# Performance work log

Hardware: AMD Instinct MI355X
Metric: run time of the kernel (lower is better)

## Reference

```python
import jax, jax.numpy as jnp
import numpy as np

K_NN = 9  # kernel_size: neighbors per node (includes self, dist 0)


def knn_edges(feat):
    """feat: (B, C, N). Replicates DenseDilatedKnnGraph (dilation=1):
    L2-normalize over channels, dense pairwise sq-distance, top-k nearest."""
    nrm = jnp.sqrt(jnp.sum(feat * feat, axis=1, keepdims=True))
    xn = feat / jnp.maximum(nrm, 1e-12)            # F.normalize(dim=1)
    xt = jnp.swapaxes(xn, 1, 2)                    # (B, N, C)
    sq = jnp.sum(xt * xt, axis=-1)                 # (B, N)
    dist = sq[:, :, None] + sq[:, None, :] - 2.0 * jnp.einsum('bnc,bmc->bnm', xt, xt)
    _, nn_idx = jax.lax.top_k(-dist, K_NN)         # (B, N, k)
    center = jnp.broadcast_to(jnp.arange(nn_idx.shape[1], dtype=nn_idx.dtype)[None, :, None], nn_idx.shape)
    return nn_idx, center                          # (x_j sources, x_i targets)


def reference(x, W0, W1, bias):
    B, C, H, W = x.shape
    N = H * W
    NB = B * N
    feat = x.reshape(B, C, N)
    # KNN graph is built on detached features in the torch source
    x_j, x_i = knn_edges(jax.lax.stop_gradient(feat))
    E = B * N * K_NN
    # faithful to source: torch.linspace(0, B, steps=E, dtype=int64) batch offsets
    count = jnp.linspace(0.0, float(B), E).astype(jnp.int32)
    src = x_j.reshape(-1).astype(jnp.int32) + count * N
    dst = x_i.reshape(-1).astype(jnp.int32) + count * N
    valid = (src < NB) & (dst < NB)                # drop the out-of-range tail edge
    # flat_nodes: (B, C, H, W) -> (B*H*W, C), node id = b*HW + pixel
    nodes = jnp.swapaxes(feat, 1, 2).reshape(NB, C)
    # ChebConv K=2, sym norm, lambda_max=2: Tx0 = x, Tx1 = -(D^-1/2 A D^-1/2) x
    w = valid.astype(nodes.dtype)
    deg = jax.ops.segment_sum(w, src, num_segments=NB)
    dinv = jnp.where(deg > 0, jax.lax.rsqrt(jnp.maximum(deg, 1.0)), 0.0)
    norm = -(dinv[src] * w * dinv[dst])            # scaled-Laplacian edge weights
    msg = norm[:, None] * nodes[src]               # (E, C) gather + weight
    Tx1 = jax.ops.segment_sum(msg, dst, num_segments=NB)
    return nodes @ W0 + Tx1 @ W1 + bias


def setup_inputs() -> dict:
    key = jax.random.key(0)
    k1, k2, k3, k4 = jax.random.split(key, 4)
    B, C, H, W = 8, 48, 64, 64
    Cout = 48
    s = 1.0 / np.sqrt(C)
    return {
        'x': jax.random.normal(k1, (B, C, H, W), dtype=jnp.float32),
        'W0': jax.random.normal(k2, (C, Cout), dtype=jnp.float32) * s,
        'W1': jax.random.normal(k3, (C, Cout), dtype=jnp.float32) * s,
        'bias': jax.random.normal(k4, (Cout,), dtype=jnp.float32) * 0.01,
    }
```

## Files before the change

### kernel.cpp

```cpp
#include <hip/hip_runtime.h>

#define BATCH 8
#define CH    48
#define NPTS  4096
#define NBN   (BATCH*NPTS)
#define KNN   9
#define NCAND 12

typedef unsigned short u16;
typedef unsigned int   u32;
typedef unsigned long long u64;
typedef __bf16 bf16x8 __attribute__((ext_vector_type(8)));
typedef float  f32x4  __attribute__((ext_vector_type(4)));

__device__ __forceinline__ float bf2f(u16 v) { return __uint_as_float(((u32)v) << 16); }
__device__ __forceinline__ u16 f2bf(float f) {
  u32 u = __float_as_uint(f);
  u = (u + 0x7fffu + ((u >> 16) & 1u)) >> 16;
  return (u16)u;
}

#define MED3U(d, a, b, c) \
  asm("v_med3_u32 %0, %1, %2, %3" : "=v"(d) : "v"(a), "v"(b), "v"(c))
#define INS12(p0,p1,p2,p3,p4,p5,p6,p7,p8,p9,p10,p11,x) do { \
  MED3U(p11,p10,p11,x); MED3U(p10,p9,p10,x); MED3U(p9,p8,p9,x);  \
  MED3U(p8, p7, p8, x); MED3U(p7, p6,p7, x); MED3U(p6,p5,p6,x);  \
  MED3U(p5, p4, p5, x); MED3U(p4, p3,p4, x); MED3U(p3,p2,p3,x);  \
  MED3U(p2, p1, p2, x); MED3U(p1, p0,p1, x); p0 = min(p0, x);    \
} while (0)

__device__ __forceinline__ void stage_q(const u16* g, u16* l) {
  __builtin_amdgcn_global_load_lds(
      (const __attribute__((address_space(1))) void*)g,
      (__attribute__((address_space(3))) void*)l, 16, 0, 0);
}

__global__ __launch_bounds__(64)
void k_prep(const float* __restrict__ x, float* __restrict__ xraw,
            float* __restrict__ xn, float* __restrict__ csq,
            u16* __restrict__ Abuf, u16* __restrict__ Bbuf,
            int* __restrict__ deg) {
  int node = blockIdx.x * 64 + threadIdx.x;
  deg[node] = 0;
  int b = node >> 12, n = node & (NPTS - 1);
  const float* xb = x + (size_t)b * CH * NPTS;
  float f[CH];
#pragma unroll
  for (int c = 0; c < CH; ++c) f[c] = xb[(size_t)c * NPTS + n];
  float a0 = 0, a1 = 0, a2 = 0, a3 = 0;
#pragma unroll
  for (int k = 0; k < CH; k += 4) {
    a0 += f[k] * f[k]; a1 += f[k+1] * f[k+1];
    a2 += f[k+2] * f[k+2]; a3 += f[k+3] * f[k+3];
  }
  float nrm = fmaxf(sqrtf((a0 + a1) + (a2 + a3)), 1e-12f);
  float rn = 1.0f / nrm;
  a0 = a1 = a2 = a3 = 0;
#pragma unroll
  for (int k = 0; k < CH; k += 4) {
    float v0 = f[k]*rn, v1 = f[k+1]*rn, v2 = f[k+2]*rn, v3 = f[k+3]*rn;
    a0 += v0*v0; a1 += v1*v1; a2 += v2*v2; a3 += v3*v3;
  }
  float csqv = (a0 + a1) + (a2 + a3);
  csq[node] = csqv;
  float4* ro = (float4*)(xraw + (size_t)node * CH);
  float4* no = (float4*)(xn   + (size_t)node * CH);
#pragma unroll
  for (int i = 0; i < CH / 4; ++i) {
    ro[i] = make_float4(f[4*i], f[4*i+1], f[4*i+2], f[4*i+3]);
    no[i] = make_float4(f[4*i]*rn, f[4*i+1]*rn, f[4*i+2]*rn, f[4*i+3]*rn);
  }
  uint4* Bo = (uint4*)(Bbuf + (size_t)node * 128);
  u16* Ag = Abuf + (size_t)(node >> 4) * 2048 + (size_t)(node & 15) * 8;
#pragma unroll
  for (int g = 0; g < 6; ++g) {
    u32 bhw[4], blw[4], ahw[4], alw[4];
#pragma unroll
    for (int j = 0; j < 4; ++j) {
      int k = g * 8 + j * 2;
      float v0 = f[k] * rn, v1 = f[k+1] * rn;
      u16 h0 = f2bf(v0), h1 = f2bf(v1);
      u16 l0 = f2bf(v0 - bf2f(h0)), l1 = f2bf(v1 - bf2f(h1));
      bhw[j] = (u32)h0 | ((u32)h1 << 16);
      blw[j] = (u32)l0 | ((u32)l1 << 16);
      float w0 = -2.0f * v0, w1 = -2.0f * v1;
      u16 g0 = f2bf(w0), g1 = f2bf(w1);
      u16 m0 = f2bf(w0 - bf2f(g0)), m1 = f2bf(w1 - bf2f(g1));
      ahw[j] = (u32)g0 | ((u32)g1 << 16);
      alw[j] = (u32)m0 | ((u32)m1 << 16);
    }
    Bo[g]     = make_uint4(bhw[0], bhw[1], bhw[2], bhw[3]);
    Bo[8 + g] = make_uint4(blw[0], blw[1], blw[2], blw[3]);
    int v = g >> 2, q = g & 3;
    *(uint4*)(Ag + v * 512 + q * 128)        = make_uint4(ahw[0], ahw[1], ahw[2], ahw[3]);
    *(uint4*)(Ag + 1024 + v * 512 + q * 128) = make_uint4(alw[0], alw[1], alw[2], alw[3]);
  }
  {
    u16 h = f2bf(csqv); u16 l = f2bf(csqv - bf2f(h));
    Bo[6]  = make_uint4(0x3F80u, 0, 0, 0);
    Bo[14] = make_uint4(0, 0, 0, 0);
    *(uint4*)(Ag + 512 + 2 * 128)        = make_uint4((u32)h, 0, 0, 0);
    *(uint4*)(Ag + 1024 + 512 + 2 * 128) = make_uint4((u32)l, 0, 0, 0);
  }
  {
    uint4 z = make_uint4(0, 0, 0, 0);
    Bo[7] = z; Bo[15] = z;
    *(uint4*)(Ag + 512 + 3 * 128)        = z;
    *(uint4*)(Ag + 1024 + 512 + 3 * 128) = z;
  }
}

__global__ __launch_bounds__(256, 6)
void k_knn_m(const u16* __restrict__ Abuf, const u16* __restrict__ Bbuf,
             u32* __restrict__ candu) {
  __shared__ __align__(16) u16 As[2][2][2048];
  int tid = threadIdx.x;
  int lane = tid & 63;
  int wv = tid >> 6;
  int quad = lane >> 4, m16 = lane & 15;
  int panel = blockIdx.x * 4 + wv;
  int row = panel * 16 + m16;
  int b4096 = row & ~(NPTS - 1);
  int half = blockIdx.y;
  int ct0 = half * 128;

  const __bf16* Bb = (const __bf16*)Bbuf + (size_t)row * 128;
  bf16x8 bh0 = *(const bf16x8*)(Bb + quad * 8);
  bf16x8 bh1 = *(const bf16x8*)(Bb + 32 + quad * 8);
  bf16x8 bl0 = *(const bf16x8*)(Bb + 64 + quad * 8);
  bf16x8 bl1 = *(const bf16x8*)(Bb + 96 + quad * 8);

  const u16* gs = Abuf + ((size_t)(b4096 >> 4) + ct0) * 2048
                  + wv * 512 + lane * 8;

  u32 s0=~0u,s1=~0u,s2=~0u,s3=~0u,s4=~0u,s5=~0u,
      s6=~0u,s7=~0u,s8=~0u,s9=~0u,s10=~0u,s11=~0u;

  const f32x4 C25 = {2.5f, 2.5f, 2.5f, 2.5f};

#define LDA(P, S, A0,A1,A2,A3) do {                                         \
    const u16* _p = &As[P][S][lane * 8];                                    \
    A0 = *(const bf16x8*)(_p);                                              \
    A1 = *(const bf16x8*)(_p + 512);                                        \
    A2 = *(const bf16x8*)(_p + 1024);                                       \
    A3 = *(const bf16x8*)(_p + 1536);                                       \
  } while (0)
#define MFMA6(ACC, A0,A1,A2,A3) do {                                        \
    ACC = __builtin_amdgcn_mfma_f32_16x16x32_bf16(A0, bh0, C25, 0, 0, 0);   \
    ACC = __builtin_amdgcn_mfma_f32_16x16x32_bf16(A1, bh1, ACC, 0, 0, 0);   \
    ACC = __builtin_amdgcn_mfma_f32_16x16x32_bf16(A0, bl0, ACC, 0, 0, 0);   \
    ACC = __builtin_amdgcn_mfma_f32_16x16x32_bf16(A1, bl1, ACC, 0, 0, 0);   \
    ACC = __builtin_amdgcn_mfma_f32_16x16x32_bf16(A2, bh0, ACC, 0, 0, 0);   \
    ACC = __builtin_amdgcn_mfma_f32_16x16x32_bf16(A3, bh1, ACC, 0, 0, 0);   \
  } while (0)
#define FILTER(ACC, CT) do {                                                \
    u32 _colb = ((u32)(CT) << 4) | ((u32)quad << 2);                        \
    _Pragma("unroll")                                                       \
    for (int _r = 0; _r < 4; ++_r) {                                        \
      u32 _u = __float_as_uint((ACC)[_r]);                                  \
      u32 _x = (_u & 0xFFFFF000u) | (_colb | (u32)_r);                      \
      INS12(s0,s1,s2,s3,s4,s5,s6,s7,s8,s9,s10,s11, _x);                     \
    }                                                                       \
  } while (0)

  f32x4 accA, accB;
  bf16x8 a0, a1, a2, a3;

  stage_q(gs,        &As[0][0][wv * 512]);
  stage_q(gs + 2048, &As[0][1][wv * 512]);
  __syncthreads();

  LDA(0, 0, a0, a1, a2, a3);
  stage_q(gs + (size_t)2 * 2048, &As[1][0][wv * 512]);
  stage_q(gs + (size_t)3 * 2048, &As[1][1][wv * 512]);
  MFMA6(accA, a0, a1, a2, a3);
  LDA(0, 1, a0, a1, a2, a3);
  MFMA6(accB, a0, a1, a2, a3);
  FILTER(accA, ct0 + 0);
  __syncthreads();

  for (int p = 1; p < 63; ++p) {
    int par = p & 1;
    LDA(par, 0, a0, a1, a2, a3);
    stage_q(gs + (size_t)(2 * p + 2) * 2048, &As[par ^ 1][0][wv * 512]);
    stage_q(gs + (size_t)(2 * p + 3) * 2048, &As[par ^ 1][1][wv * 512]);
    MFMA6(accA, a0, a1, a2, a3);
    FILTER(accB, ct0 + 2 * p - 1);
    LDA(par, 1, a0, a1, a2, a3);
    MFMA6(accB, a0, a1, a2, a3);
    FILTER(accA, ct0 + 2 * p);
    __syncthreads();
  }
  LDA(1, 0, a0, a1, a2, a3);
  MFMA6(accA, a0, a1, a2, a3);
  FILTER(accB, ct0 + 125);
  LDA(1, 1, a0, a1, a2, a3);
  MFMA6(accB, a0, a1, a2, a3);
  FILTER(accA, ct0 + 126);
  FILTER(accB, ct0 + 127);
#undef LDA
#undef MFMA6
#undef FILTER

  u32* o = candu + (((size_t)row * 2 + half) * 4 + quad) * NCAND;
  o[0]=s0; o[1]=s1; o[2]=s2; o[3]=s3; o[4]=s4; o[5]=s5;
  o[6]=s6; o[7]=s7; o[8]=s8; o[9]=s9; o[10]=s10; o[11]=s11;
}

__global__ __launch_bounds__(256, 4)
void k_reduce(const u32* __restrict__ candu, u32* __restrict__ cand12) {
  __shared__ __align__(16) u32 ls[64 * 4 * NCAND];
  int tid = threadIdx.x;
  int lr = tid >> 2, q = tid & 3;
  int row = blockIdx.x * 64 + lr;
  const uint4* src = (const uint4*)(candu + (size_t)row * 96 + q * 24);
  u32 t0=~0u,t1=~0u,t2=~0u,t3=~0u,t4=~0u,t5=~0u,
      t6=~0u,t7=~0u,t8=~0u,t9=~0u,t10=~0u,t11=~0u;
  for (int s = 0; s < 6; ++s) {
    uint4 v = src[s];
    INS12(t0,t1,t2,t3,t4,t5,t6,t7,t8,t9,t10,t11, v.x);
    INS12(t0,t1,t2,t3,t4,t5,t6,t7,t8,t9,t10,t11, v.y);
    INS12(t0,t1,t2,t3,t4,t5,t6,t7,t8,t9,t10,t11, v.z);
    INS12(t0,t1,t2,t3,t4,t5,t6,t7,t8,t9,t10,t11, v.w);
  }
  u32* lw = ls + (size_t)(lr * 4 + q) * NCAND;
  lw[0]=t0; lw[1]=t1; lw[2]=t2; lw[3]=t3; lw[4]=t4; lw[5]=t5;
  lw[6]=t6; lw[7]=t7; lw[8]=t8; lw[9]=t9; lw[10]=t10; lw[11]=t11;
  __syncthreads();
  if (q == 0) {
    u32 g0=~0u,g1=~0u,g2=~0u,g3=~0u,g4=~0u,g5=~0u,
        g6=~0u,g7=~0u,g8=~0u,g9=~0u,g10=~0u,g11=~0u;
    const uint4* lsrc = (const uint4*)(ls + (size_t)lr * 48);
    for (int s = 0; s < 12; ++s) {
      uint4 v = lsrc[s];
      INS12(g0,g1,g2,g3,g4,g5,g6,g7,g8,g9,g10,g11, v.x);
      INS12(g0,g1,g2,g3,g4,g5,g6,g7,g8,g9,g10,g11, v.y);
      INS12(g0,g1,g2,g3,g4,g5,g6,g7,g8,g9,g10,g11, v.z);
      INS12(g0,g1,g2,g3,g4,g5,g6,g7,g8,g9,g10,g11, v.w);
    }
    u32* o = cand12 + (size_t)row * NCAND;
    o[0]=(g0&0xFFFu); o[1]=(g1&0xFFFu); o[2]=(g2&0xFFFu);
    o[3]=(g3&0xFFFu); o[4]=(g4&0xFFFu); o[5]=(g5&0xFFFu);
    o[6]=(g6&0xFFFu); o[7]=(g7&0xFFFu); o[8]=(g8&0xFFFu);
    o[9]=(g9&0xFFFu); o[10]=(g10&0xFFFu); o[11]=(g11&0xFFFu);
  }
}

#define RR 16
__global__ __launch_bounds__(256, 4)
void k_rescore(const float* __restrict__ xn, const float* __restrict__ csq,
               const u32* __restrict__ cand12,
               u16* __restrict__ nn, int* __restrict__ deg) {
  __shared__ float dS[RR * NCAND];
  __shared__ int   iS[RR * NCAND];
  int tid = threadIdx.x;
  int lr = tid >> 4, q = tid & 15;
  int bi = blockIdx.x;
  int row = (bi & 7) * NPTS + (bi >> 3) * RR + lr;
  int b4096 = row & ~(NPTS - 1);
  const float* xnb = xn + (size_t)b4096 * CH;
  if (q < NCAND) {
    float rf[CH];
    const float4* p = (const float4*)(xn + (size_t)row * CH);
#pragma unroll
    for (int i = 0; i < CH / 4; ++i) {
      float4 v = p[i];
      rf[4*i] = v.x; rf[4*i+1] = v.y; rf[4*i+2] = v.z; rf[4*i+3] = v.w;
    }
    float sqn = csq[row];
    int c = (int)(cand12[(size_t)row * NCAND + q] & (NPTS - 1));
    const float4* cp = (const float4*)(xnb + (size_t)c * CH);
    float a0 = 0, a1 = 0, a2 = 0, a3 = 0;
#pragma unroll
    for (int i = 0; i < CH / 4; ++i) {
      float4 v = cp[i];
      a0 += rf[4*i]   * v.x; a1 += rf[4*i+1] * v.y;
      a2 += rf[4*i+2] * v.z; a3 += rf[4*i+3] * v.w;
    }
    float dist = (sqn + csq[b4096 + c]) - 2.0f * ((a0 + a1) + (a2 + a3));
    dS[lr * NCAND + q] = dist;
    iS[lr * NCAND + q] = c;
  }
  __syncthreads();
  if (q == 0) {
    float gd[KNN]; int gi[KNN];
#pragma unroll
    for (int j = 0; j < KNN; ++j) { gd[j] = 3.4e38f; gi[j] = 0x7fffffff; }
    for (int s = 0; s < NCAND; ++s) {
      float dc = dS[lr * NCAND + s]; int ic = iS[lr * NCAND + s];
      if (dc < gd[KNN - 1] || (dc == gd[KNN - 1] && ic < gi[KNN - 1])) {
        gd[KNN - 1] = dc; gi[KNN - 1] = ic;
#pragma unroll
        for (int k2 = KNN - 1; k2 > 0; --k2) {
          bool sw = (gd[k2] < gd[k2 - 1]) ||
                    (gd[k2] == gd[k2 - 1] && gi[k2] < gi[k2 - 1]);
          if (sw) {
            float td = gd[k2]; gd[k2] = gd[k2 - 1]; gd[k2 - 1] = td;
            int ti = gi[k2]; gi[k2] = gi[k2 - 1]; gi[k2 - 1] = ti;
          }
        }
      }
    }
    u16* o = nn + (size_t)row * KNN;
    int jmax = (row == NBN - 1) ? (KNN - 1) : KNN;
#pragma unroll
    for (int j = 0; j < KNN; ++j) o[j] = (u16)(gi[j] & (NPTS - 1));
    for (int j = 0; j < jmax; ++j)
      atomicAdd(&deg[b4096 + (gi[j] & (NPTS - 1))], 1);
  }
}

#define ONB 64
#define LPAD 52
__global__ __launch_bounds__(256)
void k_out_f(const float* __restrict__ xraw, const u16* __restrict__ nn,
             const int* __restrict__ deg,
             const float* __restrict__ W0, const float* __restrict__ W1,
             const float* __restrict__ bias, float* __restrict__ out) {
  __shared__ float w0[CH * CH], w1[CH * CH], bs[CH];
  __shared__ __align__(16) float fS[ONB * LPAD];
  __shared__ __align__(16) float txS[ONB * LPAD];
  __shared__ float dinvS[ONB];
  int tid = threadIdx.x;
  int bi = blockIdx.x;
  int n0 = (bi & 7) * NPTS + (bi >> 3) * ONB;
  int b12 = n0 & ~(NPTS - 1);
  for (int i = tid; i < CH * CH; i += 256) { w0[i] = W0[i]; w1[i] = W1[i]; }
  if (tid < CH) bs[tid] = bias[tid];
  for (int i = tid; i < ONB * 12; i += 256) {
    int ln = i / 12, f4 = i % 12;
    *(float4*)(fS + ln * LPAD + f4 * 4) =
        *(const float4*)(xraw + (size_t)(n0 + ln) * CH + f4 * 4);
  }
  if (tid < ONB) {
    int dg = deg[n0 + tid];
    dinvS[tid] = (dg > 0) ? (1.0f / sqrtf((float)dg)) : 0.0f;
  }
  __syncthreads();

  int ln = tid >> 2, p = tid & 3;
  int node = n0 + ln;
  float dn = dinvS[ln];
  const u16* nrow = nn + (size_t)node * KNN;
  bool full = (node != NBN - 1);
  float tx[12];
#pragma unroll
  for (int i = 0; i < 12; ++i) tx[i] = 0.f;
#pragma unroll
  for (int j = 0; j < KNN; ++j) {
    if (j < KNN - 1 || full) {
      int s = nrow[j] & (NPTS - 1);
      int dgs = deg[b12 + s];
      float ds = (dgs > 0) ? (1.0f / sqrtf((float)dgs)) : 0.0f;
      float w = -(ds * dn);
      const float4* pr = (const float4*)(xraw + (size_t)(b12 + s) * CH + p * 12);
#pragma unroll
      for (int q3 = 0; q3 < 3; ++q3) {
        float4 v = pr[q3];
        tx[q3*4]   += w * v.x; tx[q3*4+1] += w * v.y;
        tx[q3*4+2] += w * v.z; tx[q3*4+3] += w * v.w;
      }
    }
  }
#pragma unroll
  for (int q3 = 0; q3 < 3; ++q3)
    *(float4*)(txS + ln * LPAD + p * 12 + q3 * 4) =
        make_float4(tx[q3*4], tx[q3*4+1], tx[q3*4+2], tx[q3*4+3]);
  __syncthreads();

  float acc[12];
#pragma unroll
  for (int i = 0; i < 12; ++i) acc[i] = bs[p * 12 + i];
  const float* fr = fS + ln * LPAD;
  const float* tr = txS + ln * LPAD;
#pragma unroll
  for (int c = 0; c < CH; ++c) {
    float fc = fr[c];
    const float* wr = w0 + c * CH + p * 12;
#pragma unroll
    for (int i = 0; i < 12; ++i) acc[i] += fc * wr[i];
  }
#pragma unroll
  for (int c = 0; c < CH; ++c) {
    float tc = tr[c];
    const float* wr = w1 + c * CH + p * 12;
#pragma unroll
    for (int i = 0; i < 12; ++i) acc[i] += tc * wr[i];
  }
  float* op = out + (size_t)node * CH + p * 12;
#pragma unroll
  for (int q3 = 0; q3 < 3; ++q3)
    *(float4*)(op + q3 * 4) =
        make_float4(acc[q3*4], acc[q3*4+1], acc[q3*4+2], acc[q3*4+3]);
}

__global__ __launch_bounds__(256)
void k_zero(int* __restrict__ deg) { deg[blockIdx.x * 256 + threadIdx.x] = 0; }

__global__ __launch_bounds__(256)
void k_hist(const u16* __restrict__ nn, int* __restrict__ deg) {
  int node = blockIdx.x * 256 + threadIdx.x;
  int b12 = node & ~(NPTS - 1);
  int jmax = (node == NBN - 1) ? (KNN - 1) : KNN;
  for (int j = 0; j < jmax; ++j)
    atomicAdd(&deg[b12 + (nn[(size_t)node * KNN + j] & (NPTS - 1))], 1);
}

__global__ __launch_bounds__(256)
void k_dinv(const int* __restrict__ deg, float* __restrict__ dinv) {
  int i = blockIdx.x * 256 + threadIdx.x;
  int dg = deg[i];
  dinv[i] = (dg > 0) ? (1.0f / sqrtf((float)dg)) : 0.0f;
}

#define NQ    4
#define QCOLS (NPTS/NQ)
#define TCOLS 32
#define NTILES (QCOLS/TCOLS)
#define RPB   64

__global__ __launch_bounds__(256)
void k_knn_nb(const float* __restrict__ x, u16* __restrict__ nn) {
  __shared__ __align__(16) float tile[NQ * TCOLS * CH];
  __shared__ float nrmS[NQ * TCOLS];
  __shared__ float csq[NQ * TCOLS];
  int tid = threadIdx.x;
  int r0 = blockIdx.x * RPB;
  int b  = r0 >> 12;
  int q  = tid >> 6;
  int lr = tid & 63;
  int n  = (r0 + lr) & (NPTS - 1);
  const float* xb = x + (size_t)b * CH * NPTS;
  float rf[CH];
#pragma unroll
  for (int c = 0; c < CH; ++c) rf[c] = xb[(size_t)c * NPTS + n];
  float sqn;
  {
    float a0 = 0, a1 = 0, a2 = 0, a3 = 0;
#pragma unroll
    for (int k = 0; k < CH; k += 4) {
      a0 += rf[k] * rf[k]; a1 += rf[k+1] * rf[k+1];
      a2 += rf[k+2] * rf[k+2]; a3 += rf[k+3] * rf[k+3];
    }
    float nrm = fmaxf(sqrtf((a0 + a1) + (a2 + a3)), 1e-12f);
#pragma unroll
    for (int c = 0; c < CH; ++c) rf[c] = rf[c] / nrm;
    a0 = a1 = a2 = a3 = 0;
#pragma unroll
    for (int k = 0; k < CH; k += 4) {
      a0 += rf[k] * rf[k]; a1 += rf[k+1] * rf[k+1];
      a2 += rf[k+2] * rf[k+2]; a3 += rf[k+3] * rf[k+3];
    }
    sqn = (a0 + a1) + (a2 + a3);
  }
  float d[KNN]; int id[KNN];
#pragma unroll
  for (int j = 0; j < KNN; ++j) { d[j] = 3.4e38f; id[j] = 0x7fffffff; }
  for (int t = 0; t < NTILES; ++t) {
    __syncthreads();
#pragma unroll
    for (int qq = 0; qq < NQ; ++qq) {
      int colbase = qq * QCOLS + t * TCOLS;
      float* dst = tile + qq * TCOLS * CH;
#pragma unroll
      for (int it = 0; it < 6; ++it) {
        int i = it * 256 + tid;
        int c = i >> 5, p = i & 31;
        dst[p * CH + c] = xb[(size_t)c * NPTS + colbase + p];
      }
    }
    __syncthreads();
    if (tid < NQ * TCOLS) {
      const float* cp = tile + tid * CH;
      float a0 = 0, a1 = 0, a2 = 0, a3 = 0;
#pragma unroll
      for (int k = 0; k < CH; k += 4) {
        float4 v = *(const float4*)(cp + k);
        a0 += v.x * v.x; a1 += v.y * v.y; a2 += v.z * v.z; a3 += v.w * v.w;
      }
      nrmS[tid] = fmaxf(sqrtf((a0 + a1) + (a2 + a3)), 1e-12f);
    }
    __syncthreads();
    for (int i = tid; i < NQ * TCOLS * CH; i += 256)
      tile[i] = tile[i] / nrmS[i / CH];
    __syncthreads();
    if (tid < NQ * TCOLS) {
      const float* cp = tile + tid * CH;
      float a0 = 0, a1 = 0, a2 = 0, a3 = 0;
#pragma unroll
      for (int k = 0; k < CH; k += 4) {
        float4 v = *(const float4*)(cp + k);
        a0 += v.x * v.x; a1 += v.y * v.y; a2 += v.z * v.z; a3 += v.w * v.w;
      }
      csq[tid] = (a0 + a1) + (a2 + a3);
    }
    __syncthreads();
    int cbase = q * QCOLS + t * TCOLS;
    const float* tq = tile + q * TCOLS * CH;
    for (int cc = 0; cc < TCOLS; ++cc) {
      const float* cp = tq + cc * CH;
      float a0 = 0, a1 = 0, a2 = 0, a3 = 0;
#pragma unroll
      for (int k = 0; k < CH; k += 4) {
        float4 v = *(const float4*)(cp + k);
        a0 += rf[k] * v.x; a1 += rf[k+1] * v.y;
        a2 += rf[k+2] * v.z; a3 += rf[k+3] * v.w;
      }
      float dist = (sqn + csq[q * TCOLS + cc]) - 2.0f * ((a0 + a1) + (a2 + a3));
      if (dist < d[KNN - 1]) {
        d[KNN - 1] = dist; id[KNN - 1] = cbase + cc;
#pragma unroll
        for (int k2 = KNN - 1; k2 > 0; --k2) {
          if (d[k2] < d[k2 - 1]) {
            float td = d[k2]; d[k2] = d[k2 - 1]; d[k2 - 1] = td;
            int ti = id[k2]; id[k2] = id[k2 - 1]; id[k2 - 1] = ti;
          }
        }
      }
    }
  }
  __syncthreads();
  float* md = tile;
  int*   mi = (int*)(tile + 256 * KNN);
#pragma unroll
  for (int j = 0; j < KNN; ++j) { md[tid * KNN + j] = d[j]; mi[tid * KNN + j] = id[j]; }
  __syncthreads();
  if (tid < RPB) {
    float fd[KNN]; int fi[KNN];
#pragma unroll
    for (int j = 0; j < KNN; ++j) { fd[j] = 3.4e38f; fi[j] = 0x7fffffff; }
    for (int qq = 0; qq < NQ; ++qq) {
      int s = qq * RPB + tid;
      for (int j = 0; j < KNN; ++j) {
        float dc = md[s * KNN + j]; int ic = mi[s * KNN + j];
        if (dc < fd[KNN - 1]) {
          fd[KNN - 1] = dc; fi[KNN - 1] = ic;
#pragma unroll
          for (int k2 = KNN - 1; k2 > 0; --k2) {
            if (fd[k2] < fd[k2 - 1]) {
              float td = fd[k2]; fd[k2] = fd[k2 - 1]; fd[k2 - 1] = td;
              int ti = fi[k2]; fi[k2] = fi[k2 - 1]; fi[k2 - 1] = ti;
            }
          }
        }
      }
    }
    u16* o = nn + (size_t)(r0 + tid) * KNN;
#pragma unroll
    for (int j = 0; j < KNN; ++j) o[j] = (u16)(fi[j] & (NPTS - 1));
  }
}

__global__ __launch_bounds__(256)
void k_out_nb(const float* __restrict__ x, const u16* __restrict__ nn,
              const float* __restrict__ dinv,
              const float* __restrict__ W0, const float* __restrict__ W1,
              const float* __restrict__ bias, float* __restrict__ out) {
  __shared__ float w0[CH * CH], w1[CH * CH], bs[CH];
  for (int i = threadIdx.x; i < CH * CH; i += 256) { w0[i] = W0[i]; w1[i] = W1[i]; }
  if (threadIdx.x < CH) bs[threadIdx.x] = bias[threadIdx.x];
  __syncthreads();
  int node = blockIdx.x * 256 + threadIdx.x;
  int b = node >> 12, n = node & (NPTS - 1);
  const float* xb = x + (size_t)b * CH * NPTS;
  float f[CH], acc[CH], tx[CH];
#pragma unroll
  for (int c = 0; c < CH; ++c) f[c] = xb[(size_t)c * NPTS + n];
#pragma unroll
  for (int o = 0; o < CH; ++o) acc[o] = bs[o];
#pragma unroll
  for (int c = 0; c < CH; ++c) {
    float fc = f[c];
    const float* wr = w0 + c * CH;
#pragma unroll
    for (int o = 0; o < CH; ++o) acc[o] += fc * wr[o];
  }
#pragma unroll
  for (int c = 0; c < CH; ++c) tx[c] = 0.f;
  float dn = dinv[node];
  int jmax = (node == NBN - 1) ? (KNN - 1) : KNN;
  for (int j = 0; j < jmax; ++j) {
    int s = nn[(size_t)node * KNN + j] & (NPTS - 1);
    float w = -(dinv[(b << 12) + s] * dn);
#pragma unroll
    for (int c = 0; c < CH; ++c) tx[c] += w * xb[(size_t)c * NPTS + s];
  }
#pragma unroll
  for (int c = 0; c < CH; ++c) {
    float tc = tx[c];
    const float* wr = w1 + c * CH;
#pragma unroll
    for (int o = 0; o < CH; ++o) acc[o] += tc * wr[o];
  }
  float4* op = (float4*)(out + (size_t)node * CH);
#pragma unroll
  for (int i = 0; i < CH / 4; ++i)
    op[i] = make_float4(acc[4*i], acc[4*i+1], acc[4*i+2], acc[4*i+3]);
}

extern "C" void kernel_launch(void* const* d_in, const int* in_sizes, int n_in,
                              void* d_out, int out_size, void* d_ws, size_t ws_size,
                              hipStream_t stream) {
  const float* x    = (const float*)d_in[0];
  const float* W0   = (const float*)d_in[1];
  const float* W1   = (const float*)d_in[2];
  const float* bias = (const float*)d_in[3];
  float* out = (float*)d_out;
  char* w = (char*)d_ws;

  const size_t SZ_XN   = (size_t)NBN * CH * 4;
  const size_t SZ_XRAW = (size_t)NBN * CH * 4;
  const size_t SZ_CSQ  = (size_t)NBN * 4;
  const size_t SZ_NN   = (size_t)NBN * KNN * 2;
  const size_t SZ_DEG  = (size_t)NBN * 4;
  const size_t SZ_AB   = (size_t)NBN * 128 * 2;
  const size_t SZ_CU   = (size_t)NBN * 8 * NCAND * 4;
  const size_t SZ_C12  = (size_t)NBN * NCAND * 4;
  const size_t needF = SZ_XN + SZ_XRAW + SZ_CSQ + SZ_NN + SZ_DEG
                     + 2 * SZ_AB + SZ_CU + SZ_C12;

  if (ws_size >= needF) {
    size_t off = 0;
    float* xn   = (float*)(w + off); off += SZ_XN;
    float* xraw = (float*)(w + off); off += SZ_XRAW;
    float* csq  = (float*)(w + off); off += SZ_CSQ;
    u16*   nn   = (u16*)  (w + off); off += SZ_NN;
    int*   deg  = (int*)  (w + off); off += SZ_DEG;
    u16*   Abuf = (u16*)  (w + off); off += SZ_AB;
    u16*   Bbuf = (u16*)  (w + off); off += SZ_AB;
    u32*   candu= (u32*)  (w + off); off += SZ_CU;
    u32*   cand12=(u32*)  (w + off);
    k_prep    <<<NBN / 64, 64, 0, stream>>>(x, xraw, xn, csq, Abuf, Bbuf, deg);
    k_knn_m   <<<dim3(NBN / 64, 2), 256, 0, stream>>>(Abuf, Bbuf, candu);
    k_reduce  <<<NBN / 64, 256, 0, stream>>>(candu, cand12);
    k_rescore <<<NBN / RR, 256, 0, stream>>>(xn, csq, cand12, nn, deg);
    k_out_f   <<<NBN / ONB, 256, 0, stream>>>(xraw, nn, deg, W0, W1, bias, out);
  } else {
    u16*   nn   = (u16*)w;
    int*   deg  = (int*)(w + SZ_NN);
    float* dinv = (float*)(w + SZ_NN + SZ_DEG);
    k_knn_nb <<<NBN / RPB, 256, 0, stream>>>(x, nn);
    k_zero   <<<NBN / 256, 256, 0, stream>>>(deg);
    k_hist   <<<NBN / 256, 256, 0, stream>>>(nn, deg);
    k_dinv   <<<NBN / 256, 256, 0, stream>>>(deg, dinv);
    k_out_nb <<<NBN / 256, 256, 0, stream>>>(x, nn, dinv, W0, W1, bias, out);
  }
}
```

Measured before the change: 206.7 us.

## Fuse candidate reduce and rescore kernels; halve output block node tile

```diff
diff --git a/kernel.cpp b/kernel.cpp
--- a/kernel.cpp
+++ b/kernel.cpp
@@ -207,69 +207,66 @@
   o[6]=s6; o[7]=s7; o[8]=s8; o[9]=s9; o[10]=s10; o[11]=s11;
 }
 
-__global__ __launch_bounds__(256, 4)
-void k_reduce(const u32* __restrict__ candu, u32* __restrict__ cand12) {
-  __shared__ __align__(16) u32 ls[64 * 4 * NCAND];
-  int tid = threadIdx.x;
-  int lr = tid >> 2, q = tid & 3;
-  int row = blockIdx.x * 64 + lr;
-  const uint4* src = (const uint4*)(candu + (size_t)row * 96 + q * 24);
-  u32 t0=~0u,t1=~0u,t2=~0u,t3=~0u,t4=~0u,t5=~0u,
-      t6=~0u,t7=~0u,t8=~0u,t9=~0u,t10=~0u,t11=~0u;
-  for (int s = 0; s < 6; ++s) {
-    uint4 v = src[s];
-    INS12(t0,t1,t2,t3,t4,t5,t6,t7,t8,t9,t10,t11, v.x);
-    INS12(t0,t1,t2,t3,t4,t5,t6,t7,t8,t9,t10,t11, v.y);
-    INS12(t0,t1,t2,t3,t4,t5,t6,t7,t8,t9,t10,t11, v.z);
-    INS12(t0,t1,t2,t3,t4,t5,t6,t7,t8,t9,t10,t11, v.w);
-  }
-  u32* lw = ls + (size_t)(lr * 4 + q) * NCAND;
-  lw[0]=t0; lw[1]=t1; lw[2]=t2; lw[3]=t3; lw[4]=t4; lw[5]=t5;
-  lw[6]=t6; lw[7]=t7; lw[8]=t8; lw[9]=t9; lw[10]=t10; lw[11]=t11;
-  __syncthreads();
-  if (q == 0) {
+#define RWS 32
+__global__ __launch_bounds__(256)
+void k_rr(const u32* __restrict__ candu, const float* __restrict__ xn,
+          const float* __restrict__ csq, u16* __restrict__ nn,
+          int* __restrict__ deg) {
+  __shared__ __align__(16) u32 cs[RWS][48];
+  __shared__ __align__(16) float xnS[RWS][52];
+  __shared__ float csqS[RWS];
+  __shared__ float dS[RWS][12];
+  __shared__ int   iS[RWS][12];
+  int tid = threadIdx.x, bi = blockIdx.x;
+  int row0 = (bi & 7) * NPTS + (bi >> 3) * RWS;
+  int b4096 = row0 & ~(NPTS - 1);
+  for (int i = tid; i < RWS * 12; i += 256) {
+    int ln = i / 12, f4 = i % 12;
+    *(float4*)&xnS[ln][f4 * 4] =
+        *(const float4*)(xn + (size_t)(row0 + ln) * CH + f4 * 4);
+  }
+  if (tid < RWS) csqS[tid] = csq[row0 + tid];
+  if (tid < RWS * 4) {
+    int lr = tid >> 2, q = tid & 3;
+    const uint4* src = (const uint4*)(candu + (size_t)(row0 + lr) * 96 + q * 24);
+    u32 t0=~0u,t1=~0u,t2=~0u,t3=~0u,t4=~0u,t5=~0u,
+        t6=~0u,t7=~0u,t8=~0u,t9=~0u,t10=~0u,t11=~0u;
+#pragma unroll
+    for (int s = 0; s < 6; ++s) {
+      uint4 v = src[s];
+      INS12(t0,t1,t2,t3,t4,t5,t6,t7,t8,t9,t10,t11, v.x);
+      INS12(t0,t1,t2,t3,t4,t5,t6,t7,t8,t9,t10,t11, v.y);
+      INS12(t0,t1,t2,t3,t4,t5,t6,t7,t8,t9,t10,t11, v.z);
+      INS12(t0,t1,t2,t3,t4,t5,t6,t7,t8,t9,t10,t11, v.w);
+    }
+    u32* lw = &cs[lr][q * 12];
+    lw[0]=t0; lw[1]=t1; lw[2]=t2; lw[3]=t3; lw[4]=t4; lw[5]=t5;
+    lw[6]=t6; lw[7]=t7; lw[8]=t8; lw[9]=t9; lw[10]=t10; lw[11]=t11;
+  }
+  __syncthreads();
+  if (tid < RWS) {
+    int lr = tid;
     u32 g0=~0u,g1=~0u,g2=~0u,g3=~0u,g4=~0u,g5=~0u,
         g6=~0u,g7=~0u,g8=~0u,g9=~0u,g10=~0u,g11=~0u;
-    const uint4* lsrc = (const uint4*)(ls + (size_t)lr * 48);
+    const uint4* ls4 = (const uint4*)&cs[lr][0];
+#pragma unroll
     for (int s = 0; s < 12; ++s) {
-      uint4 v = lsrc[s];
+      uint4 v = ls4[s];
       INS12(g0,g1,g2,g3,g4,g5,g6,g7,g8,g9,g10,g11, v.x);
       INS12(g0,g1,g2,g3,g4,g5,g6,g7,g8,g9,g10,g11, v.y);
       INS12(g0,g1,g2,g3,g4,g5,g6,g7,g8,g9,g10,g11, v.z);
       INS12(g0,g1,g2,g3,g4,g5,g6,g7,g8,g9,g10,g11, v.w);
     }
-    u32* o = cand12 + (size_t)row * NCAND;
-    o[0]=(g0&0xFFFu); o[1]=(g1&0xFFFu); o[2]=(g2&0xFFFu);
-    o[3]=(g3&0xFFFu); o[4]=(g4&0xFFFu); o[5]=(g5&0xFFFu);
-    o[6]=(g6&0xFFFu); o[7]=(g7&0xFFFu); o[8]=(g8&0xFFFu);
-    o[9]=(g9&0xFFFu); o[10]=(g10&0xFFFu); o[11]=(g11&0xFFFu);
-  }
-}
-
-#define RR 16
-__global__ __launch_bounds__(256, 4)
-void k_rescore(const float* __restrict__ xn, const float* __restrict__ csq,
-               const u32* __restrict__ cand12,
-               u16* __restrict__ nn, int* __restrict__ deg) {
-  __shared__ float dS[RR * NCAND];
-  __shared__ int   iS[RR * NCAND];
-  int tid = threadIdx.x;
-  int lr = tid >> 4, q = tid & 15;
-  int bi = blockIdx.x;
-  int row = (bi & 7) * NPTS + (bi >> 3) * RR + lr;
-  int b4096 = row & ~(NPTS - 1);
-  const float* xnb = xn + (size_t)b4096 * CH;
-  if (q < NCAND) {
-    float rf[CH];
-    const float4* p = (const float4*)(xn + (size_t)row * CH);
-#pragma unroll
-    for (int i = 0; i < CH / 4; ++i) {
-      float4 v = p[i];
-      rf[4*i] = v.x; rf[4*i+1] = v.y; rf[4*i+2] = v.z; rf[4*i+3] = v.w;
-    }
-    float sqn = csq[row];
-    int c = (int)(cand12[(size_t)row * NCAND + q] & (NPTS - 1));
-    const float4* cp = (const float4*)(xnb + (size_t)c * CH);
+    u32* lw = &cs[lr][0];
+    lw[0]=g0; lw[1]=g1; lw[2]=g2; lw[3]=g3; lw[4]=g4; lw[5]=g5;
+    lw[6]=g6; lw[7]=g7; lw[8]=g8; lw[9]=g9; lw[10]=g10; lw[11]=g11;
+  }
+  __syncthreads();
+  for (int task = tid; task < RWS * 12; task += 256) {
+    int r = task / 12, j = task % 12;
+    int c = (int)(cs[r][j] & 0xFFFu);
+    const float4* cp = (const float4*)(xn + (size_t)(b4096 + c) * CH);
+    const float* rf = &xnS[r][0];
     float a0 = 0, a1 = 0, a2 = 0, a3 = 0;
 #pragma unroll
     for (int i = 0; i < CH / 4; ++i) {
@@ -277,17 +274,18 @@
       a0 += rf[4*i]   * v.x; a1 += rf[4*i+1] * v.y;
       a2 += rf[4*i+2] * v.z; a3 += rf[4*i+3] * v.w;
     }
-    float dist = (sqn + csq[b4096 + c]) - 2.0f * ((a0 + a1) + (a2 + a3));
-    dS[lr * NCAND + q] = dist;
-    iS[lr * NCAND + q] = c;
-  }
-  __syncthreads();
-  if (q == 0) {
+    float dist = (csqS[r] + csq[b4096 + c]) - 2.0f * ((a0 + a1) + (a2 + a3));
+    dS[r][j] = dist; iS[r][j] = c;
+  }
+  __syncthreads();
+  if (tid < RWS) {
+    int lr = tid;
+    int row = row0 + lr;
     float gd[KNN]; int gi[KNN];
 #pragma unroll
     for (int j = 0; j < KNN; ++j) { gd[j] = 3.4e38f; gi[j] = 0x7fffffff; }
     for (int s = 0; s < NCAND; ++s) {
-      float dc = dS[lr * NCAND + s]; int ic = iS[lr * NCAND + s];
+      float dc = dS[lr][s]; int ic = iS[lr][s];
       if (dc < gd[KNN - 1] || (dc == gd[KNN - 1] && ic < gi[KNN - 1])) {
         gd[KNN - 1] = dc; gi[KNN - 1] = ic;
 #pragma unroll
@@ -310,7 +308,7 @@
   }
 }
 
-#define ONB 64
+#define ONB 32
 #define LPAD 52
 __global__ __launch_bounds__(256)
 void k_out_f(const float* __restrict__ xraw, const u16* __restrict__ nn,
@@ -338,14 +336,14 @@
   }
   __syncthreads();
 
-  int ln = tid >> 2, p = tid & 3;
+  int ln = tid >> 3, p = tid & 7;
   int node = n0 + ln;
   float dn = dinvS[ln];
   const u16* nrow = nn + (size_t)node * KNN;
   bool full = (node != NBN - 1);
-  float tx[12];
-#pragma unroll
-  for (int i = 0; i < 12; ++i) tx[i] = 0.f;
+  float tx[6];
+#pragma unroll
+  for (int i = 0; i < 6; ++i) tx[i] = 0.f;
 #pragma unroll
   for (int j = 0; j < KNN; ++j) {
     if (j < KNN - 1 || full) {
@@ -353,45 +351,43 @@
       int dgs = deg[b12 + s];
       float ds = (dgs > 0) ? (1.0f / sqrtf((float)dgs)) : 0.0f;
       float w = -(ds * dn);
-      const float4* pr = (const float4*)(xraw + (size_t)(b12 + s) * CH + p * 12);
+      const float2* pr = (const float2*)(xraw + (size_t)(b12 + s) * CH + p * 6);
 #pragma unroll
       for (int q3 = 0; q3 < 3; ++q3) {
-        float4 v = pr[q3];
-        tx[q3*4]   += w * v.x; tx[q3*4+1] += w * v.y;
-        tx[q3*4+2] += w * v.z; tx[q3*4+3] += w * v.w;
+        float2 v = pr[q3];
+        tx[q3*2]   += w * v.x; tx[q3*2+1] += w * v.y;
       }
     }
   }
 #pragma unroll
   for (int q3 = 0; q3 < 3; ++q3)
-    *(float4*)(txS + ln * LPAD + p * 12 + q3 * 4) =
-        make_float4(tx[q3*4], tx[q3*4+1], tx[q3*4+2], tx[q3*4+3]);
-  __syncthreads();
-
-  float acc[12];
-#pragma unroll
-  for (int i = 0; i < 12; ++i) acc[i] = bs[p * 12 + i];
+    *(float2*)(txS + ln * LPAD + p * 6 + q3 * 2) =
+        make_float2(tx[q3*2], tx[q3*2+1]);
+  __syncthreads();
+
+  float acc[6];
+#pragma unroll
+  for (int i = 0; i < 6; ++i) acc[i] = bs[p * 6 + i];
   const float* fr = fS + ln * LPAD;
   const float* tr = txS + ln * LPAD;
 #pragma unroll
   for (int c = 0; c < CH; ++c) {
     float fc = fr[c];
-    const float* wr = w0 + c * CH + p * 12;
-#pragma unroll
-    for (int i = 0; i < 12; ++i) acc[i] += fc * wr[i];
+    const float* wr = w0 + c * CH + p * 6;
+#pragma unroll
+    for (int i = 0; i < 6; ++i) acc[i] += fc * wr[i];
   }
 #pragma unroll
   for (int c = 0; c < CH; ++c) {
     float tc = tr[c];
-    const float* wr = w1 + c * CH + p * 12;
-#pragma unroll
-    for (int i = 0; i < 12; ++i) acc[i] += tc * wr[i];
-  }
-  float* op = out + (size_t)node * CH + p * 12;
+    const float* wr = w1 + c * CH + p * 6;
+#pragma unroll
+    for (int i = 0; i < 6; ++i) acc[i] += tc * wr[i];
+  }
+  float* op = out + (size_t)node * CH + p * 6;
 #pragma unroll
   for (int q3 = 0; q3 < 3; ++q3)
-    *(float4*)(op + q3 * 4) =
-        make_float4(acc[q3*4], acc[q3*4+1], acc[q3*4+2], acc[q3*4+3]);
+    *(float2*)(op + q3 * 2) = make_float2(acc[q3*2], acc[q3*2+1]);
 }
 
 __global__ __launch_bounds__(256)
@@ -615,9 +611,8 @@
   const size_t SZ_DEG  = (size_t)NBN * 4;
   const size_t SZ_AB   = (size_t)NBN * 128 * 2;
   const size_t SZ_CU   = (size_t)NBN * 8 * NCAND * 4;
-  const size_t SZ_C12  = (size_t)NBN * NCAND * 4;
   const size_t needF = SZ_XN + SZ_XRAW + SZ_CSQ + SZ_NN + SZ_DEG
-                     + 2 * SZ_AB + SZ_CU + SZ_C12;
+                     + 2 * SZ_AB + SZ_CU;
 
   if (ws_size >= needF) {
     size_t off = 0;
@@ -628,12 +623,10 @@
     int*   deg  = (int*)  (w + off); off += SZ_DEG;
     u16*   Abuf = (u16*)  (w + off); off += SZ_AB;
     u16*   Bbuf = (u16*)  (w + off); off += SZ_AB;
-    u32*   candu= (u32*)  (w + off); off += SZ_CU;
-    u32*   cand12=(u32*)  (w + off);
+    u32*   candu= (u32*)  (w + off);
     k_prep    <<<NBN / 64, 64, 0, stream>>>(x, xraw, xn, csq, Abuf, Bbuf, deg);
     k_knn_m   <<<dim3(NBN / 64, 2), 256, 0, stream>>>(Abuf, Bbuf, candu);
-    k_reduce  <<<NBN / 64, 256, 0, stream>>>(candu, cand12);
-    k_rescore <<<NBN / RR, 256, 0, stream>>>(xn, csq, cand12, nn, deg);
+    k_rr      <<<NBN / RWS, 256, 0, stream>>>(candu, xn, csq, nn, deg);
     k_out_f   <<<NBN / ONB, 256, 0, stream>>>(xraw, nn, deg, W0, W1, bias, out);
   } else {
     u16*   nn   = (u16*)w;
```

Result: faster. 200.9 us (-2.8%).
